# Kernel optimization log

Measured on AMD Instinct MI355X. Metric: run time of the kernel, lower is better.

Reference implementation:

```python
import jax, jax.numpy as jnp
import numpy as np

B, N, DIM = 64, 784, 256
N1, N2, HS, WS, M, D = 1, 4, 28, 7, 8, 2  # x_windows, y_windows, H_sp, W_sp, num_heads, d
HW = HS * WS                              # 196 tokens per window
C = DIM // M                              # 32 channels per head


def setup_inputs() -> dict:
    key = jax.random.key(0)
    ks = jax.random.split(key, 5)
    x = jax.random.normal(ks[0], (B, N, DIM), dtype=jnp.float32)
    Wc = jax.random.normal(ks[1], (DIM, M * D), dtype=jnp.float32) * 0.02
    bc = jax.random.normal(ks[2], (M * D,), dtype=jnp.float32) * 0.02
    Wg = jax.random.normal(ks[3], (HW * D, HW * HW), dtype=jnp.float32) * 0.02
    bg = jax.random.normal(ks[4], (HW * HW,), dtype=jnp.float32) * 0.02
    return {"x": x, "Wc": Wc, "bc": bc, "Wg": Wg, "bg": bg}


def reference(x, Wc, bc, Wg, bg):
    b = x.shape[0]
    # compress: B N C -> B N (m d)
    w = x @ Wc + bc
    # rearrange 'b (n1 h n2 w) (m d) -> b (n1 n2 m) (h w d)'
    w = w.reshape(b, N1, HS, N2, WS, M, D)
    w = w.transpose(0, 1, 3, 5, 2, 4, 6).reshape(b, N1 * N2 * M, HW * D)
    # generate per-window mixing weights: B Nw (HW*HW)
    w = w @ Wg + bg
    w = w.reshape(b, N1 * N2 * M, HW, HW)
    # softmax over dim=-2 (the (h1 w1) source axis)
    w = jax.nn.softmax(w, axis=-2)
    # rearrange x: 'b (n1 h1 n2 w1) (m c) -> b (n1 n2 m) c (h1 w1)'
    xv = x.reshape(b, N1, HS, N2, WS, M, C)
    xv = xv.transpose(0, 1, 3, 5, 6, 2, 4).reshape(b, N1 * N2 * M, C, HW)
    # windowed mixing matmul: (b, Nw, C, HW) @ (b, Nw, HW, HW)
    out = jnp.matmul(xv, w)
    # rearrange back: 'b (n1 n2 m) c (h2 w2) -> b (n1 h2 n2 w2) (m c)'
    out = out.reshape(b, N1, N2, M, C, HS, WS)
    out = out.transpose(0, 1, 5, 2, 6, 3, 4).reshape(b, N1 * HS * N2 * WS, M * C)
    return out
```

## Files before the change

### kernel.cpp

```cpp
#include <hip/hip_runtime.h>
#include <hip/hip_bf16.h>
#include <stdint.h>
#include <stddef.h>

#define NB    64
#define NTOK  784
#define DIMC  256
#define NN2   4
#define NM    8
#define NHW   196
#define NWIN  32
#define NROWS 2048
#define NK    392
#define NKP   448
#define NBIG  38416
#define NIP   200
#define STROW 39200
#define STROW2 39232
#define NPT   39424
#define NTT   307
#define PTS   232

typedef __attribute__((ext_vector_type(4))) float f32x4;
typedef __attribute__((ext_vector_type(8))) short bf16x8;

static __device__ __forceinline__ float bf2f(unsigned short u) {
  union { unsigned int i; float f; } v; v.i = ((unsigned int)u) << 16; return v.f;
}
static __device__ __forceinline__ unsigned short f2bf(float f) {
  union { float f; unsigned int i; } v; v.f = f;
  unsigned int r = v.i + 0x7fffu + ((v.i >> 16) & 1u);
  return (unsigned short)(r >> 16);
}

__global__ __launch_bounds__(256) void k_compress(
    const float* __restrict__ x, const float* __restrict__ Wc,
    const float* __restrict__ bc, unsigned short* __restrict__ Abf) {
  __shared__ float wcs[16 * 256];
  __shared__ float bcs[16];
  const int tid = threadIdx.x;
  const int b  = blockIdx.x / NN2;
  const int n2 = blockIdx.x % NN2;
  for (int idx = tid; idx < 4096; idx += 256) {
    int c = idx >> 4, md = idx & 15;
    wcs[md * 256 + c] = Wc[idx];
  }
  if (tid < 16) bcs[tid] = bc[tid];
  __syncthreads();
  if (tid < NHW) {
    const int h = tid / 7, wcol = tid % 7;
    const int t = h * 28 + n2 * 7 + wcol;
    const float* xp = x + ((size_t)b * NTOK + t) * DIMC;
    float acc[16];
    #pragma unroll
    for (int md = 0; md < 16; ++md) acc[md] = bcs[md];
    for (int c = 0; c < 256; c += 4) {
      const f32x4 xv = *(const f32x4*)(xp + c);
      #pragma unroll
      for (int md = 0; md < 16; ++md) {
        const f32x4 wv = *(const f32x4*)(wcs + md * 256 + c);
        acc[md] += xv[0]*wv[0] + xv[1]*wv[1] + xv[2]*wv[2] + xv[3]*wv[3];
      }
    }
    #pragma unroll
    for (int md = 0; md < 16; ++md) {
      const int m = md >> 1, d = md & 1;
      const int r = b * NWIN + n2 * NM + m;
      Abf[(size_t)r * NKP + tid * 2 + d] = f2bf(acc[md]);
    }
  }
  for (int e = tid; e < NM * (NKP - NK); e += 256) {
    const int m = e / (NKP - NK);
    const int k = NK + (e % (NKP - NK));
    const int r = b * NWIN + n2 * NM + m;
    Abf[(size_t)r * NKP + k] = (k == NK) ? (unsigned short)0x3F80 : 0;
  }
}

__global__ __launch_bounds__(256) void k_wgt(
    const float* __restrict__ Wg, const float* __restrict__ bg,
    unsigned short* __restrict__ Wgbt) {
  __shared__ float tile[64][65];
  const int bid = blockIdx.x;
  const int n0 = (bid % 601) * 64;
  const int k0 = (bid / 601) * 64;
  const int tid = threadIdx.x;
  for (int idx = tid; idx < 4096; idx += 256) {
    const int kk = idx >> 6, nn = idx & 63;
    const int k = k0 + kk, n = n0 + nn;
    float v = 0.f;
    if (n < NBIG) {
      if (k < NK) v = Wg[(size_t)k * NBIG + n];
      else if (k == NK) v = bg[n];
    }
    tile[nn][kk] = v;
  }
  __syncthreads();
  for (int idx = tid; idx < 512; idx += 256) {
    const int nn = idx >> 3, gg = idx & 7;
    const int n = n0 + nn;
    if (n < NBIG) {
      const int i = n / NHW, j = n - (n / NHW) * NHW;
      const int np = j * NIP + i;
      unsigned short u8[8];
      #pragma unroll
      for (int e = 0; e < 8; ++e) u8[e] = f2bf(tile[nn][gg * 8 + e]);
      *(uint4*)&Wgbt[(size_t)np * NKP + k0 + gg * 8] = *(const uint4*)u8;
    }
  }
}

__global__ __launch_bounds__(256) void k_zero(unsigned short* __restrict__ Wgbt) {
  const int bid = blockIdx.x;
  int np;
  if (bid < 784) { const int j = bid >> 2, i = 196 + (bid & 3); np = j * NIP + i; }
  else           { np = STROW + (bid - 784); }
  unsigned int* p = (unsigned int*)(Wgbt + (size_t)np * NKP);
  if (threadIdx.x < 224) p[threadIdx.x] = 0u;
}

__global__ __launch_bounds__(512, 4) void k_gemm(
    const unsigned short* __restrict__ A,
    const unsigned short* __restrict__ Bt,
    unsigned short* __restrict__ E, int mtiles) {
  __shared__ __align__(128) short smem[32768];
  const int tid = threadIdx.x;
  const int w = tid >> 6, lane = tid & 63;
  const int nwg = gridDim.x;
  const int q = nwg >> 3, rr = nwg & 7;
  const int xcd = blockIdx.x & 7, pos = blockIdx.x >> 3;
  const int wg = (xcd < rr ? xcd * (q + 1) : rr * (q + 1) + (xcd - rr) * q) + pos;
  const int nt = wg / mtiles, mt = wg % mtiles;
  const int m0 = mt * 128, n0 = nt * 128;
  const int wm = (w >> 2) * 64, wn = (w & 3) * 32;
  const int lrow = lane >> 3;
  const int lcolsw = ((lane & 7) ^ lrow) * 8;

  const unsigned short* Arow = A  + (size_t)(m0 + w * 16 + lrow) * NKP + lcolsw;
  const unsigned short* Brow = Bt + (size_t)(n0 + w * 16 + lrow) * NKP + lcolsw;

  auto stage = [&](int kt, int buf) {
    #pragma unroll
    for (int is = 0; is < 2; ++is) {
      const int gg = w * 2 + is;
      __builtin_amdgcn_global_load_lds(
          (const __attribute__((address_space(1))) void*)(Arow + (size_t)is * 8 * NKP + kt),
          (__attribute__((address_space(3))) void*)((char*)smem + buf * 16384 + gg * 1024), 16, 0, 0);
      __builtin_amdgcn_global_load_lds(
          (const __attribute__((address_space(1))) void*)(Brow + (size_t)is * 8 * NKP + kt),
          (__attribute__((address_space(3))) void*)((char*)smem + 32768 + buf * 16384 + gg * 1024), 16, 0, 0);
    }
  };

  f32x4 acc[4][2] = {};
  stage(0, 0);
  __syncthreads();
  const int lq = lane >> 4;
  const int lx = (lane & 7);
  for (int t = 0; t < 7; ++t) {
    const int buf = t & 1;
    if (t < 6) stage((t + 1) * 64, buf ^ 1);
    const short* ab = smem + buf * 8192;
    const short* bb = smem + 16384 + buf * 8192;
    #pragma unroll
    for (int kk = 0; kk < 2; ++kk) {
      const int slot = ((kk * 4 + lq) ^ lx) * 8;
      bf16x8 af[4], bfr[2];
      #pragma unroll
      for (int i = 0; i < 4; ++i)
        af[i] = *(const bf16x8*)(ab + (wm + i * 16 + (lane & 15)) * 64 + slot);
      #pragma unroll
      for (int n = 0; n < 2; ++n)
        bfr[n] = *(const bf16x8*)(bb + (wn + n * 16 + (lane & 15)) * 64 + slot);
      #pragma unroll
      for (int mi = 0; mi < 4; ++mi)
        #pragma unroll
        for (int ni = 0; ni < 2; ++ni)
          acc[mi][ni] = __builtin_amdgcn_mfma_f32_16x16x32_bf16(af[mi], bfr[ni], acc[mi][ni], 0, 0, 0);
    }
    __syncthreads();
  }

  const int cq = lane >> 4, cr = lane & 15;
  #pragma unroll
  for (int mi = 0; mi < 4; ++mi)
    #pragma unroll
    for (int ni = 0; ni < 2; ++ni)
      #pragma unroll
      for (int e = 0; e < 4; ++e) {
        const int rl = wm + mi * 16 + cq * 4 + e;
        const int cl = wn + ni * 16 + cr;
        smem[rl * 132 + cl] = (short)f2bf(__expf(acc[mi][ni][e]));
      }
  __syncthreads();
  for (int idx = tid; idx < 2048; idx += 512) {
    const int rl = idx >> 4, seg = idx & 15;
    const int col0 = n0 + seg * 8;
    if (col0 < STROW2) {
      const uint4 v = *(const uint4*)&smem[rl * 132 + seg * 8];
      *(uint4*)&E[(size_t)(m0 + rl) * STROW2 + col0] = v;
    }
  }
}

__global__ __launch_bounds__(512) void k_mix(
    const unsigned short* __restrict__ E, const float* __restrict__ x,
    float* __restrict__ out, int row0) {
  __shared__ unsigned short Elds[22528];
  __shared__ unsigned short xvT[32 * PTS];
  const int tid = threadIdx.x, w = tid >> 6, lane = tid & 63;
  const int row = blockIdx.x >> 1, jh = blockIdx.x & 1;
  const int r = row0 + row;
  const int b = r >> 5, win = r & 31, n2 = win >> 3, m = win & 7;

  const unsigned short* Eb = E + (size_t)row * STROW2;
  const int g0 = jh ? 2800 : 0;
  const int nch = jh ? 33 : 44;
  for (int ch = w; ch < nch; ch += 8) {
    const int gr = g0 + ch * 64 + lane;
    if (gr < 4904)
      __builtin_amdgcn_global_load_lds(
          (const __attribute__((address_space(1))) void*)(Eb + (size_t)gr * 8),
          (__attribute__((address_space(3))) void*)((char*)Elds + ch * 1024), 16, 0, 0);
  }

  for (int idx = tid; idx < 1568; idx += 512) {
    const int i = idx >> 3, c4 = (idx & 7) * 4;
    const int t = (i / 7) * 28 + n2 * 7 + (i % 7);
    const f32x4 v = *(const f32x4*)(x + ((size_t)b * NTOK + t) * DIMC + m * 32 + c4);
    xvT[(c4 + 0) * PTS + i] = f2bf(v[0]);
    xvT[(c4 + 1) * PTS + i] = f2bf(v[1]);
    xvT[(c4 + 2) * PTS + i] = f2bf(v[2]);
    xvT[(c4 + 3) * PTS + i] = f2bf(v[3]);
  }
  for (int idx = tid; idx < 32 * (PTS - NHW); idx += 512) {
    const int c = idx / (PTS - NHW), i = NHW + idx % (PTS - NHW);
    xvT[c * PTS + i] = 0;
  }
  __syncthreads();

  bf16x8 bfr[2][7];
  #pragma unroll
  for (int ct = 0; ct < 2; ++ct)
    #pragma unroll
    for (int kk = 0; kk < 7; ++kk)
      bfr[ct][kk] = *(const bf16x8*)&xvT[(ct * 16 + (lane & 15)) * PTS + kk * 32 + (lane >> 4) * 8];
  const bool den = (lane & 15) == 0;
  bf16x8 oneA, oneB;
  #pragma unroll
  for (int e = 0; e < 8; ++e) {
    oneA[e] = den ? (short)0x3F80 : (short)0;
    const int i6 = 192 + (lane >> 4) * 8 + e;
    oneB[e] = (den && i6 < NHW) ? (short)0x3F80 : (short)0;
  }

  const int jt0 = jh ? 7 : 0;
  const int jtend = jh ? 13 : 7;
  for (int jt = jt0 + w; jt < jtend; jt += 8) {
    const int jA = jt * 16 + (lane & 15);
    const int jAc = (jA < NHW) ? jA : NHW - 1;
    const unsigned short* rp = Elds + jAc * NIP - jh * 22400 + (lane >> 4) * 8;
    bf16x8 af[7];
    #pragma unroll
    for (int kk = 0; kk < 7; ++kk) af[kk] = *(const bf16x8*)(rp + kk * 32);
    f32x4 a0 = {0.f,0.f,0.f,0.f}, a1 = {0.f,0.f,0.f,0.f}, ad = {0.f,0.f,0.f,0.f};
    #pragma unroll
    for (int kk = 0; kk < 7; ++kk) {
      a0 = __builtin_amdgcn_mfma_f32_16x16x32_bf16(af[kk], bfr[0][kk], a0, 0, 0, 0);
      a1 = __builtin_amdgcn_mfma_f32_16x16x32_bf16(af[kk], bfr[1][kk], a1, 0, 0, 0);
      ad = __builtin_amdgcn_mfma_f32_16x16x32_bf16(af[kk], (kk < 6) ? oneA : oneB, ad, 0, 0, 0);
    }
    const int c = lane & 15;
    #pragma unroll
    for (int e = 0; e < 4; ++e) {
      const int j = jt * 16 + (lane >> 4) * 4 + e;
      const float dv = __shfl(ad[e], lane & 48);
      if (j < NHW) {
        const float inv = 1.f / dv;
        const int t2 = (j / 7) * 28 + n2 * 7 + (j % 7);
        float* op = out + ((size_t)b * NTOK + t2) * DIMC + m * 32;
        op[c] = a0[e] * inv;
        op[c + 16] = a1[e] * inv;
      }
    }
  }
}

extern "C" void kernel_launch(void* const* d_in, const int* in_sizes, int n_in,
                              void* d_out, int out_size, void* d_ws, size_t ws_size,
                              hipStream_t stream) {
  const float* x  = (const float*)d_in[0];
  const float* Wc = (const float*)d_in[1];
  const float* bc = (const float*)d_in[2];
  const float* Wg = (const float*)d_in[3];
  const float* bg = (const float*)d_in[4];
  float* out = (float*)d_out;

  char* ws = (char*)d_ws;
  const size_t wgbt_bytes = (size_t)NPT * NKP * 2;
  const size_t a_bytes    = (size_t)NROWS * NKP * 2;
  unsigned short* Wgbt = (unsigned short*)ws;
  unsigned short* Abf  = (unsigned short*)(ws + wgbt_bytes);
  unsigned short* E    = (unsigned short*)(ws + wgbt_bytes + a_bytes);
  const size_t fixed = wgbt_bytes + a_bytes;
  const size_t srow_bytes = (size_t)STROW2 * 2;

  size_t avail = (ws_size > fixed) ? (ws_size - fixed) : 0;
  int rows_chunk = (int)(avail / srow_bytes);
  rows_chunk = (rows_chunk / 128) * 128;
  if (rows_chunk > 1024) rows_chunk = 1024;
  if (rows_chunk < 128)  rows_chunk = 128;

  hipLaunchKernelGGL(k_compress, dim3(NB * NN2), dim3(256), 0, stream, x, Wc, bc, Abf);
  hipLaunchKernelGGL(k_wgt, dim3(601 * 7), dim3(256), 0, stream, Wg, bg, Wgbt);
  hipLaunchKernelGGL(k_zero, dim3(1008), dim3(256), 0, stream, Wgbt);
  for (int row0 = 0; row0 < NROWS; row0 += rows_chunk) {
    int rc = NROWS - row0; if (rc > rows_chunk) rc = rows_chunk;
    hipLaunchKernelGGL(k_gemm, dim3((rc / 128) * NTT), dim3(512), 0, stream,
                       Abf + (size_t)row0 * NKP, Wgbt, E, rc / 128);
    hipLaunchKernelGGL(k_mix, dim3(rc * 2), dim3(512), 0, stream, E, x, out, row0);
  }
}
```

Measured before the change: 217.1 us.

## Fuse GEMM and mix into one kernel, overlapping chunk pipeline with double-buffered E

Merges the GEMM and mixing kernels into one launch in which interleaved blocks either compute the exp-GEMM for chunk c or run the mix for chunk c-1. The E buffer is double-buffered so the two stages can overlap. The aim is to remove the launch tail and serialization between GEMM and mix and to let memory-bound mix work overlap with compute-bound GEMM work. In exchange, the fused kernel drops the occupancy hint of 4 blocks per CU, shares one LDS footprint between both roles, and shrinks the chunk size, which means more launches.

```diff
diff --git a/kernel.cpp b/kernel.cpp
--- a/kernel.cpp
+++ b/kernel.cpp
@@ -119,16 +119,13 @@
   if (threadIdx.x < 224) p[threadIdx.x] = 0u;
 }
 
-__global__ __launch_bounds__(512, 4) void k_gemm(
-    const unsigned short* __restrict__ A,
-    const unsigned short* __restrict__ Bt,
+static __device__ __forceinline__ void gemm_body(
+    short* smem, int role, int nwg, int tid,
+    const unsigned short* __restrict__ A, const unsigned short* __restrict__ Bt,
     unsigned short* __restrict__ E, int mtiles) {
-  __shared__ __align__(128) short smem[32768];
-  const int tid = threadIdx.x;
   const int w = tid >> 6, lane = tid & 63;
-  const int nwg = gridDim.x;
   const int q = nwg >> 3, rr = nwg & 7;
-  const int xcd = blockIdx.x & 7, pos = blockIdx.x >> 3;
+  const int xcd = role & 7, pos = role >> 3;
   const int wg = (xcd < rr ? xcd * (q + 1) : rr * (q + 1) + (xcd - rr) * q) + pos;
   const int nt = wg / mtiles, mt = wg % mtiles;
   const int m0 = mt * 128, n0 = nt * 128;
@@ -203,13 +200,14 @@
   }
 }
 
-__global__ __launch_bounds__(512) void k_mix(
+static __device__ __forceinline__ void mix_body(
+    short* smem, int role, int tid,
     const unsigned short* __restrict__ E, const float* __restrict__ x,
     float* __restrict__ out, int row0) {
-  __shared__ unsigned short Elds[22528];
-  __shared__ unsigned short xvT[32 * PTS];
-  const int tid = threadIdx.x, w = tid >> 6, lane = tid & 63;
-  const int row = blockIdx.x >> 1, jh = blockIdx.x & 1;
+  unsigned short* Elds = (unsigned short*)smem;
+  unsigned short* xvT  = (unsigned short*)smem + 22528;
+  const int w = tid >> 6, lane = tid & 63;
+  const int row = role >> 1, jh = role & 1;
   const int r = row0 + row;
   const int b = r >> 5, win = r & 31, n2 = win >> 3, m = win & 7;
 
@@ -286,6 +284,29 @@
   }
 }
 
+__global__ __launch_bounds__(512) void k_fused(
+    const unsigned short* __restrict__ A, const unsigned short* __restrict__ Bt,
+    unsigned short* __restrict__ Ew, int mtiles, int gemmBlocks,
+    const unsigned short* __restrict__ Er, const float* __restrict__ x,
+    float* __restrict__ out, int row0_prev, int mixBlocks) {
+  __shared__ __align__(128) short smem[32768];
+  const int bid = blockIdx.x;
+  const int tid = threadIdx.x;
+  if ((bid & 1) && (bid >> 1) < mixBlocks) {
+    mix_body(smem, bid >> 1, tid, Er, x, out, row0_prev);
+  } else {
+    const int role = (bid < 2 * mixBlocks) ? (bid >> 1) : bid - mixBlocks;
+    gemm_body(smem, role, gemmBlocks, tid, A, Bt, Ew, mtiles);
+  }
+}
+
+__global__ __launch_bounds__(512) void k_mix(
+    const unsigned short* __restrict__ E, const float* __restrict__ x,
+    float* __restrict__ out, int row0) {
+  __shared__ __align__(128) short smem[32768];
+  mix_body(smem, blockIdx.x, threadIdx.x, E, x, out, row0);
+}
+
 extern "C" void kernel_launch(void* const* d_in, const int* in_sizes, int n_in,
                               void* d_out, int out_size, void* d_ws, size_t ws_size,
                               hipStream_t stream) {
@@ -306,18 +327,23 @@
   const size_t srow_bytes = (size_t)STROW2 * 2;
 
   size_t avail = (ws_size > fixed) ? (ws_size - fixed) : 0;
-  int rows_chunk = (int)(avail / srow_bytes);
-  rows_chunk = (rows_chunk / 128) * 128;
-  if (rows_chunk > 1024) rows_chunk = 1024;
-  if (rows_chunk < 128)  rows_chunk = 128;
+  int CH = 512;
+  while (CH > 128 && (size_t)2 * CH * srow_bytes > avail) CH >>= 1;
+  const size_t eoff = (size_t)CH * STROW2;
 
   hipLaunchKernelGGL(k_compress, dim3(NB * NN2), dim3(256), 0, stream, x, Wc, bc, Abf);
   hipLaunchKernelGGL(k_wgt, dim3(601 * 7), dim3(256), 0, stream, Wg, bg, Wgbt);
   hipLaunchKernelGGL(k_zero, dim3(1008), dim3(256), 0, stream, Wgbt);
-  for (int row0 = 0; row0 < NROWS; row0 += rows_chunk) {
-    int rc = NROWS - row0; if (rc > rows_chunk) rc = rows_chunk;
-    hipLaunchKernelGGL(k_gemm, dim3((rc / 128) * NTT), dim3(512), 0, stream,
-                       Abf + (size_t)row0 * NKP, Wgbt, E, rc / 128);
-    hipLaunchKernelGGL(k_mix, dim3(rc * 2), dim3(512), 0, stream, E, x, out, row0);
-  }
-}
+
+  const int nch = NROWS / CH;
+  const int gemmBlocks = (CH / 128) * NTT;
+  for (int c = 0; c < nch; ++c) {
+    const int mixBlocks = (c > 0) ? CH * 2 : 0;
+    hipLaunchKernelGGL(k_fused, dim3(gemmBlocks + mixBlocks), dim3(512), 0, stream,
+                       Abf + (size_t)c * CH * NKP, Wgbt, E + (c & 1) * eoff,
+                       CH / 128, gemmBlocks,
+                       E + ((c - 1) & 1) * eoff, x, out, (c - 1) * CH, mixBlocks);
+  }
+  hipLaunchKernelGGL(k_mix, dim3(CH * 2), dim3(512), 0, stream,
+                     E + ((nch - 1) & 1) * eoff, x, out, (nch - 1) * CH);
+}
```

New measurement: 250.4 us. 15.4% more time.
